# Performance work log

Measured on AMD Instinct MI355X. Metric: run time of the kernel, lower is better.

Reference implementation:

```python
import jax, jax.numpy as jnp
import numpy as np
from jax import lax

N_STATES = 512
VOCAB = 32000
BATCH = 16
SEQ_LEN = 128


def setup_inputs() -> dict:
    key = jax.random.key(0)
    k_ids, k_em, k_tm, k_p = jax.random.split(key, 4)
    input_ids = jax.random.randint(k_ids, (BATCH, SEQ_LEN), 0, VOCAB, dtype=jnp.int64)
    em = jax.random.normal(k_em, (N_STATES, VOCAB), dtype=jnp.float32)
    tm = jax.random.normal(k_tm, (N_STATES, N_STATES), dtype=jnp.float32)
    p = jax.random.normal(k_p, (N_STATES,), dtype=jnp.float32)
    return {"input_ids": input_ids, "em": em, "tm": tm, "p": p}


def reference(input_ids, em, tm, p):
    """HMM forward algorithm in log space; returns mean NLL (scalar).

    em: [S, V] emission logits, tm: [S, S] transition logits, p: [S] prior logits.
    do_log_softmax=True -> normalize each in log space first.
    """
    log_em = jax.nn.log_softmax(em, axis=-1)   # [S, V]
    log_tm = jax.nn.log_softmax(tm, axis=-1)   # [S, S] rows = source state
    log_p = jax.nn.log_softmax(p, axis=-1)     # [S]

    # Gather emission log-probs per token: [B, T, S]
    em_tok = log_em.T[input_ids]

    # alpha_0[b, s] = log_p[s] + log_em[s, x_0]
    alpha0 = log_p[None, :] + em_tok[:, 0]     # [B, S]

    def step(alpha, e_t):
        # alpha: [B, S_src]; log-matmul: logsumexp over source states
        a = jax.nn.logsumexp(alpha[:, :, None] + log_tm[None, :, :], axis=1) + e_t
        return a, None

    em_rest = jnp.swapaxes(em_tok[:, 1:], 0, 1)  # [T-1, B, S]
    alpha_T, _ = lax.scan(step, alpha0, em_rest)

    # loss = -mean_b log p(x_b) = -mean_b logsumexp_s alpha_T[b, s]
    loss = -jnp.mean(jax.nn.logsumexp(alpha_T, axis=-1))
    return loss
```

## Files before the change

kernel.cpp:

```cpp
#include <hip/hip_runtime.h>
#include <hip/hip_bf16.h>

#define NS 512
#define NV 32000
#define NB 16
#define NT 128

#ifndef __has_builtin
#define __has_builtin(x) 0
#endif

typedef int v8i __attribute__((ext_vector_type(8)));
typedef float v4f __attribute__((ext_vector_type(4)));

__device__ inline unsigned enc_e4m3(float x) {
    x = fminf(x, 448.0f);
    unsigned u = __float_as_uint(x);
    if (x < 0.015625f) {
        return (unsigned)(int)rintf(x * 512.0f);
    }
    unsigned u2 = u + 0x7FFFFu + ((u >> 20) & 1u);
    return (((u2 >> 23) - 120u) << 3) | ((u2 >> 20) & 7u);
}

__device__ inline unsigned pack4_e4m3(float a, float b, float c, float d) {
#if __has_builtin(__builtin_amdgcn_cvt_pk_fp8_f32)
    int v = __builtin_amdgcn_cvt_pk_fp8_f32(a, b, 0, false);
    v = __builtin_amdgcn_cvt_pk_fp8_f32(c, d, v, true);
    return (unsigned)v;
#else
    return enc_e4m3(a) | (enc_e4m3(b) << 8) | (enc_e4m3(c) << 16) | (enc_e4m3(d) << 24);
#endif
}

#define DPPMAX(x, ctrl) \
    x = fmaxf(x, __int_as_float(__builtin_amdgcn_mov_dpp(__float_as_int(x), ctrl, 0xF, 0xF, true)))
#define DPPADD(x, ctrl) \
    x = x + __int_as_float(__builtin_amdgcn_mov_dpp(__float_as_int(x), ctrl, 0xF, 0xF, true))

__global__ __launch_bounds__(256) void k_emtok_T(
    const float* __restrict__ em, const int* __restrict__ ids,
    float* __restrict__ em_lin_T)
{
    const int s   = blockIdx.x;
    const int tid = threadIdx.x;
    const float* row = em + (size_t)s * NV;

    float sum = 0.f;
    const float4* row4 = (const float4*)row;
#pragma unroll 4
    for (int i = 0; i < 31; ++i) {
        float4 v = row4[tid + 256 * i];
        sum += __expf(v.x) + __expf(v.y) + __expf(v.z) + __expf(v.w);
    }
    sum += __expf(row[31744 + tid]);

#pragma unroll
    for (int off = 32; off; off >>= 1) sum += __shfl_down(sum, off);
    __shared__ float red[4];
    __shared__ float s_scale;
    if ((tid & 63) == 0) red[tid >> 6] = sum;
    __syncthreads();
    if (tid == 0) s_scale = (1.0f / ((red[0] + red[1]) + (red[2] + red[3]))) * 0x1p-18f;
    __syncthreads();
    const float scale = s_scale;

    for (int j = tid; j < NB * NT; j += 256) {
        em_lin_T[(size_t)s * (NB * NT) + j] = __expf(row[ids[j]]) * scale;
    }
}

__global__ __launch_bounds__(256) void k_emtok_direct(
    const float* __restrict__ em, const int* __restrict__ ids,
    float* __restrict__ em_lin)
{
    const int s   = blockIdx.x;
    const int tid = threadIdx.x;
    const float* row = em + (size_t)s * NV;

    float sum = 0.f;
    const float4* row4 = (const float4*)row;
#pragma unroll 4
    for (int i = 0; i < 31; ++i) {
        float4 v = row4[tid + 256 * i];
        sum += __expf(v.x) + __expf(v.y) + __expf(v.z) + __expf(v.w);
    }
    sum += __expf(row[31744 + tid]);
#pragma unroll
    for (int off = 32; off; off >>= 1) sum += __shfl_down(sum, off);
    __shared__ float red[4];
    __shared__ float s_scale;
    if ((tid & 63) == 0) red[tid >> 6] = sum;
    __syncthreads();
    if (tid == 0) s_scale = (1.0f / ((red[0] + red[1]) + (red[2] + red[3]))) * 0x1p-18f;
    __syncthreads();
    const float scale = s_scale;
    for (int j = tid; j < NB * NT; j += 256) {
        em_lin[(size_t)j * NS + s] = __expf(row[ids[j]]) * scale;
    }
}

__global__ __launch_bounds__(256) void k_tr(
    const float* __restrict__ emT, float* __restrict__ em_lin)
{
    __shared__ float tile[32][33];
    const int jb = blockIdx.x * 32;
    const int sb = blockIdx.y * 32;
    const int cc = threadIdx.x & 31;
    const int rr = threadIdx.x >> 5;
#pragma unroll
    for (int i = 0; i < 4; ++i) {
        int r = rr + 8 * i;
        tile[r][cc] = emT[(size_t)(sb + r) * (NB * NT) + jb + cc];
    }
    __syncthreads();
#pragma unroll
    for (int i = 0; i < 4; ++i) {
        int r = rr + 8 * i;
        em_lin[(size_t)(jb + r) * NS + sb + cc] = tile[cc][r];
    }
}

__global__ __launch_bounds__(64) void k_pt(
    const float* __restrict__ tm, unsigned char* __restrict__ PT)
{
    const int k    = blockIdx.x;
    const int lane = threadIdx.x;
    const float* row = tm + (size_t)k * NS;

    float4 a = ((const float4*)row)[lane * 2];
    float4 b = ((const float4*)row)[lane * 2 + 1];
    float e0 = __expf(a.x), e1 = __expf(a.y), e2 = __expf(a.z), e3 = __expf(a.w);
    float e4 = __expf(b.x), e5 = __expf(b.y), e6 = __expf(b.z), e7 = __expf(b.w);
    float sum = ((e0 + e1) + (e2 + e3)) + ((e4 + e5) + (e6 + e7));
#pragma unroll
    for (int off = 32; off; off >>= 1) sum += __shfl_down(sum, off);
    sum = __shfl(sum, 0);
    const float sc = 1024.0f / sum;

    float ev[8] = {e0, e1, e2, e3, e4, e5, e6, e7};
#pragma unroll
    for (int i = 0; i < 8; ++i) {
        int d = lane * 8 + i;
        PT[(size_t)d * NS + k] = (unsigned char)(pack4_e4m3(ev[i] * sc, 0.f, 0.f, 0.f) & 0xFFu);
    }
}

__global__ __launch_bounds__(512, 2) void k_scan(
    const float* __restrict__ em_lin, const unsigned char* __restrict__ PT,
    const float* __restrict__ p, float* __restrict__ out)
{
    const int tid = threadIdx.x;
    const int w   = tid >> 6;
    const int l   = tid & 63;
    const int lc  = l & 15;
    const int lq  = l >> 4;

    __shared__ unsigned int Ew[2][16 * 128];
    __shared__ float wm[16][8];
    __shared__ float mbuf[16];
    __shared__ int   sbuf[16];

    v8i B[4][4];
#pragma unroll
    for (int nt = 0; nt < 4; ++nt) {
#pragma unroll
        for (int kt = 0; kt < 4; ++kt) {
            const uint4* src = (const uint4*)(PT + (size_t)((w * 4 + nt) * 16 + lc) * NS + kt * 128 + lq * 32);
            uint4 lo = src[0], hi = src[1];
            v8i bb;
            bb[0] = (int)lo.x; bb[1] = (int)lo.y; bb[2] = (int)lo.z; bb[3] = (int)lo.w;
            bb[4] = (int)hi.x; bb[5] = (int)hi.y; bb[6] = (int)hi.z; bb[7] = (int)hi.w;
            B[nt][kt] = bb;
        }
    }

    float zp = 0.f;
#pragma unroll
    for (int i = 0; i < 8; ++i) zp += __expf(p[l * 8 + i]);
    DPPADD(zp, 0x111); DPPADD(zp, 0x112); DPPADD(zp, 0x114); DPPADD(zp, 0x118);
    float Zp = __int_as_float(__builtin_amdgcn_readlane(__float_as_int(zp), 15))
             + __int_as_float(__builtin_amdgcn_readlane(__float_as_int(zp), 31))
             + __int_as_float(__builtin_amdgcn_readlane(__float_as_int(zp), 47))
             + __int_as_float(__builtin_amdgcn_readlane(__float_as_int(zp), 63));
    const float invZp = 1.0f / Zp;

    int dbase[4];
#pragma unroll
    for (int nt = 0; nt < 4; ++nt) dbase[nt] = (w * 4 + nt) * 16 + lc;

    float alpha[4][4];
#pragma unroll
    for (int nt = 0; nt < 4; ++nt) {
        float pl = __expf(p[dbase[nt]]) * invZp;
#pragma unroll
        for (int r = 0; r < 4; ++r)
            alpha[nt][r] = pl * em_lin[(4 * lq + r) * (NT * NS) + dbase[nt]];
    }

    int shift[4] = {0, 0, 0, 0};
    const unsigned sel1 = (l & 1) ? 0x07030501u : 0x02060004u;
    const unsigned sel2 = (l & 2) ? 0x07060302u : 0x01000504u;
    const int mrow = 4 * lq + (l & 3);

    for (int t = 1; t < NT; ++t) {
        float epf[4][4];
#pragma unroll
        for (int nt = 0; nt < 4; ++nt)
#pragma unroll
            for (int r = 0; r < 4; ++r)
                epf[nt][r] = em_lin[(4 * lq + r) * (NT * NS) + t * NS + dbase[nt]];

#pragma unroll
        for (int r = 0; r < 4; ++r) {
            float mx = fmaxf(fmaxf(alpha[0][r], alpha[1][r]), fmaxf(alpha[2][r], alpha[3][r]));
            DPPMAX(mx, 0x111); DPPMAX(mx, 0x112); DPPMAX(mx, 0x114); DPPMAX(mx, 0x118);
            if (lc == 15) wm[4 * lq + r][w] = mx;
        }
        __syncthreads();
        if (w == 0 && l < 16) {
            float4 a = *(const float4*)&wm[l][0];
            float4 b = *(const float4*)&wm[l][4];
            mbuf[l] = fmaxf(fmaxf(fmaxf(a.x, a.y), fmaxf(a.z, a.w)),
                            fmaxf(fmaxf(b.x, b.y), fmaxf(b.z, b.w)));
        }
        __syncthreads();
        float4 mb4 = *(const float4*)&mbuf[4 * lq];
        float mbv[4] = {mb4.x, mb4.y, mb4.z, mb4.w};
        float sc[4];
#pragma unroll
        for (int r = 0; r < 4; ++r) {
            int Eb = (int)(__float_as_uint(mbv[r]) >> 23);
            sc[r] = __uint_as_float((unsigned)(261 - Eb) << 23);
            shift[r] += Eb - 126;
        }
#pragma unroll
        for (int nt = 0; nt < 4; ++nt) {
            unsigned dw = pack4_e4m3(alpha[nt][0] * sc[0], alpha[nt][1] * sc[1],
                                     alpha[nt][2] * sc[2], alpha[nt][3] * sc[3]);
            int tmp = __builtin_amdgcn_mov_dpp((int)dw, 0xB1, 0xF, 0xF, true);
            dw = __builtin_amdgcn_perm(dw, (unsigned)tmp, sel1);
            tmp = __builtin_amdgcn_mov_dpp((int)dw, 0x4E, 0xF, 0xF, true);
            dw = __builtin_amdgcn_perm(dw, (unsigned)tmp, sel2);
            int chunk = ((w * 4 + nt) ^ mrow) & 31;
            Ew[t & 1][mrow * 128 + chunk * 4 + (lc >> 2)] = dw;
        }
        __syncthreads();

        v8i A[4];
        const uint4* eb = (const uint4*)&Ew[t & 1][0];
#pragma unroll
        for (int kt = 0; kt < 4; ++kt) {
            uint4 lo = eb[lc * 32 + (((kt * 8 + lq * 2 + 0) ^ lc) & 31)];
            uint4 hi = eb[lc * 32 + (((kt * 8 + lq * 2 + 1) ^ lc) & 31)];
            v8i aa;
            aa[0] = (int)lo.x; aa[1] = (int)lo.y; aa[2] = (int)lo.z; aa[3] = (int)lo.w;
            aa[4] = (int)hi.x; aa[5] = (int)hi.y; aa[6] = (int)hi.z; aa[7] = (int)hi.w;
            A[kt] = aa;
        }

        v4f C[4];
#pragma unroll
        for (int nt = 0; nt < 4; ++nt) { C[nt][0] = 0.f; C[nt][1] = 0.f; C[nt][2] = 0.f; C[nt][3] = 0.f; }
#pragma unroll
        for (int kt = 0; kt < 4; ++kt)
#pragma unroll
            for (int nt = 0; nt < 4; ++nt)
                C[nt] = __builtin_amdgcn_mfma_scale_f32_16x16x128_f8f6f4(
                            A[kt], B[nt][kt], C[nt], 0, 0, 0, 0x7F7F7F7F, 0, 0x7F7F7F7F);

#pragma unroll
        for (int nt = 0; nt < 4; ++nt)
#pragma unroll
            for (int r = 0; r < 4; ++r)
                alpha[nt][r] = C[nt][r] * epf[nt][r];
    }

#pragma unroll
    for (int r = 0; r < 4; ++r) {
        float sm = ((alpha[0][r] + alpha[1][r]) + (alpha[2][r] + alpha[3][r]));
        DPPADD(sm, 0x111); DPPADD(sm, 0x112); DPPADD(sm, 0x114); DPPADD(sm, 0x118);
        if (lc == 15) wm[4 * lq + r][w] = sm;
        if (w == 0 && lc == 0) sbuf[4 * lq + r] = shift[r];
    }
    __syncthreads();
    if (w == 0 && l < 16) {
        float4 a = *(const float4*)&wm[l][0];
        float4 b = *(const float4*)&wm[l][4];
        float s8 = ((a.x + a.y) + (a.z + a.w)) + ((b.x + b.y) + (b.z + b.w));
        float L2 = __log2f(s8) + (float)sbuf[l];
        DPPADD(L2, 0x111); DPPADD(L2, 0x112); DPPADD(L2, 0x114); DPPADD(L2, 0x118);
        if (l == 15) out[0] = -(0.693147180559945f / 16.0f) * L2;
    }
}

extern "C" void kernel_launch(void* const* d_in, const int* in_sizes, int n_in,
                              void* d_out, int out_size, void* d_ws, size_t ws_size,
                              hipStream_t stream)
{
    const int*   ids = (const int*)d_in[0];
    const float* em  = (const float*)d_in[1];
    const float* tm  = (const float*)d_in[2];
    const float* p   = (const float*)d_in[3];
    float* out = (float*)d_out;

    float*          em_lin = (float*)d_ws;
    unsigned char*  PT     = (unsigned char*)d_ws + ((size_t)4 << 20);
    float*          emT    = (float*)((unsigned char*)d_ws + ((size_t)4 << 20) + ((size_t)256 << 10));

    const bool big_ws = ws_size >= (((size_t)8 << 20) + ((size_t)512 << 10));

    if (big_ws) {
        k_emtok_T<<<NS, 256, 0, stream>>>(em, ids, emT);
        k_tr<<<dim3(64, 16), 256, 0, stream>>>(emT, em_lin);
    } else {
        k_emtok_direct<<<NS, 256, 0, stream>>>(em, ids, em_lin);
    }
    k_pt<<<NS, 64, 0, stream>>>(tm, PT);
    k_scan<<<1, 512, 0, stream>>>(em_lin, PT, p, out);
}
```

Before: 295.7 us.

## Drop a scan barrier per step, coalesce PT build, prefetch emission gathers

In the serial scan, every thread now reads all eight per-warp maxima from shared memory and reduces them itself, which removes one __syncthreads per timestep. The Ew exchange buffer becomes single-buffered, and the emission pointers are advanced incrementally instead of being recomputed. The transition-matrix fp8 transpose is split into a row-normaliser kernel and a tiled kernel that writes coalesced 16-byte stores, replacing byte-wise strided writes. The emission gather values are loaded before the softmax-sum loop so their latency overlaps it. The trade-offs are one extra kernel launch and redundant max reductions in every thread, and the initial shift value changes to 18.

```diff
diff --git a/kernel.cpp b/kernel.cpp
--- a/kernel.cpp
+++ b/kernel.cpp
@@ -46,6 +46,13 @@
     const int tid = threadIdx.x;
     const float* row = em + (size_t)s * NV;
 
+    int idv[8];
+#pragma unroll
+    for (int k = 0; k < 8; ++k) idv[k] = ids[tid + 256 * k];
+    float g[8];
+#pragma unroll
+    for (int k = 0; k < 8; ++k) g[k] = row[idv[k]];
+
     float sum = 0.f;
     const float4* row4 = (const float4*)row;
 #pragma unroll 4
@@ -65,9 +72,9 @@
     __syncthreads();
     const float scale = s_scale;
 
-    for (int j = tid; j < NB * NT; j += 256) {
-        em_lin_T[(size_t)s * (NB * NT) + j] = __expf(row[ids[j]]) * scale;
-    }
+#pragma unroll
+    for (int k = 0; k < 8; ++k)
+        em_lin_T[(size_t)s * (NB * NT) + tid + 256 * k] = __expf(g[k]) * scale;
 }
 
 __global__ __launch_bounds__(256) void k_emtok_direct(
@@ -77,6 +84,13 @@
     const int s   = blockIdx.x;
     const int tid = threadIdx.x;
     const float* row = em + (size_t)s * NV;
+
+    int idv[8];
+#pragma unroll
+    for (int k = 0; k < 8; ++k) idv[k] = ids[tid + 256 * k];
+    float g[8];
+#pragma unroll
+    for (int k = 0; k < 8; ++k) g[k] = row[idv[k]];
 
     float sum = 0.f;
     const float4* row4 = (const float4*)row;
@@ -95,9 +109,9 @@
     if (tid == 0) s_scale = (1.0f / ((red[0] + red[1]) + (red[2] + red[3]))) * 0x1p-18f;
     __syncthreads();
     const float scale = s_scale;
-    for (int j = tid; j < NB * NT; j += 256) {
-        em_lin[(size_t)j * NS + s] = __expf(row[ids[j]]) * scale;
-    }
+#pragma unroll
+    for (int k = 0; k < 8; ++k)
+        em_lin[(size_t)(tid + 256 * k) * NS + s] = __expf(g[k]) * scale;
 }
 
 __global__ __launch_bounds__(256) void k_tr(
@@ -121,8 +135,8 @@
     }
 }
 
-__global__ __launch_bounds__(64) void k_pt(
-    const float* __restrict__ tm, unsigned char* __restrict__ PT)
+__global__ __launch_bounds__(64) void k_z(
+    const float* __restrict__ tm, float* __restrict__ zscale)
 {
     const int k    = blockIdx.x;
     const int lane = threadIdx.x;
@@ -130,20 +144,46 @@
 
     float4 a = ((const float4*)row)[lane * 2];
     float4 b = ((const float4*)row)[lane * 2 + 1];
-    float e0 = __expf(a.x), e1 = __expf(a.y), e2 = __expf(a.z), e3 = __expf(a.w);
-    float e4 = __expf(b.x), e5 = __expf(b.y), e6 = __expf(b.z), e7 = __expf(b.w);
-    float sum = ((e0 + e1) + (e2 + e3)) + ((e4 + e5) + (e6 + e7));
+    float sum = ((__expf(a.x) + __expf(a.y)) + (__expf(a.z) + __expf(a.w)))
+              + ((__expf(b.x) + __expf(b.y)) + (__expf(b.z) + __expf(b.w)));
 #pragma unroll
     for (int off = 32; off; off >>= 1) sum += __shfl_down(sum, off);
-    sum = __shfl(sum, 0);
-    const float sc = 1024.0f / sum;
-
-    float ev[8] = {e0, e1, e2, e3, e4, e5, e6, e7};
-#pragma unroll
-    for (int i = 0; i < 8; ++i) {
-        int d = lane * 8 + i;
-        PT[(size_t)d * NS + k] = (unsigned char)(pack4_e4m3(ev[i] * sc, 0.f, 0.f, 0.f) & 0xFFu);
-    }
+    if (lane == 0) zscale[k] = 1024.0f / sum;
+}
+
+__global__ __launch_bounds__(256) void k_pt2(
+    const float* __restrict__ tm, const float* __restrict__ zscale,
+    unsigned char* __restrict__ PT)
+{
+    __shared__ float tile[64][65];
+    __shared__ float zs[64];
+    const int kb  = blockIdx.x * 64;
+    const int db  = blockIdx.y * 64;
+    const int tid = threadIdx.x;
+    const int c   = tid & 63;
+    const int r0  = tid >> 6;
+
+    if (tid < 64) zs[tid] = zscale[kb + tid];
+#pragma unroll
+    for (int i = 0; i < 16; ++i) {
+        int r = r0 + 4 * i;
+        tile[r][c] = tm[(size_t)(kb + r) * NS + db + c];
+    }
+    __syncthreads();
+
+    const int d  = tid >> 2;
+    const int ks = (tid & 3) * 16;
+    unsigned px[4];
+#pragma unroll
+    for (int gq = 0; gq < 4; ++gq) {
+        int k0 = ks + gq * 4;
+        px[gq] = pack4_e4m3(__expf(tile[k0 + 0][d]) * zs[k0 + 0],
+                            __expf(tile[k0 + 1][d]) * zs[k0 + 1],
+                            __expf(tile[k0 + 2][d]) * zs[k0 + 2],
+                            __expf(tile[k0 + 3][d]) * zs[k0 + 3]);
+    }
+    uint4 o; o.x = px[0]; o.y = px[1]; o.z = px[2]; o.w = px[3];
+    *(uint4*)(PT + (size_t)(db + d) * NS + kb + ks) = o;
 }
 
 __global__ __launch_bounds__(512, 2) void k_scan(
@@ -156,9 +196,8 @@
     const int lc  = l & 15;
     const int lq  = l >> 4;
 
-    __shared__ unsigned int Ew[2][16 * 128];
-    __shared__ float wm[16][8];
-    __shared__ float mbuf[16];
+    __shared__ unsigned int Ew[16 * 128];
+    __shared__ float wm2[8][16];
     __shared__ int   sbuf[16];
 
     v8i B[4][4];
@@ -185,48 +224,65 @@
              + __int_as_float(__builtin_amdgcn_readlane(__float_as_int(zp), 63));
     const float invZp = 1.0f / Zp;
 
-    int dbase[4];
-#pragma unroll
-    for (int nt = 0; nt < 4; ++nt) dbase[nt] = (w * 4 + nt) * 16 + lc;
+    const int dbase0 = w * 64 + lc;
 
     float alpha[4][4];
 #pragma unroll
     for (int nt = 0; nt < 4; ++nt) {
-        float pl = __expf(p[dbase[nt]]) * invZp;
+        float pl = __expf(p[dbase0 + 16 * nt]) * invZp;
 #pragma unroll
         for (int r = 0; r < 4; ++r)
-            alpha[nt][r] = pl * em_lin[(4 * lq + r) * (NT * NS) + dbase[nt]];
-    }
-
-    int shift[4] = {0, 0, 0, 0};
+            alpha[nt][r] = pl * em_lin[(4 * lq + r) * (NT * NS) + dbase0 + 16 * nt];
+    }
+
+    int shift[4] = {18, 18, 18, 18};
     const unsigned sel1 = (l & 1) ? 0x07030501u : 0x02060004u;
     const unsigned sel2 = (l & 2) ? 0x07060302u : 0x01000504u;
     const int mrow = 4 * lq + (l & 3);
 
+    const float* ep[4];
+#pragma unroll
+    for (int r = 0; r < 4; ++r)
+        ep[r] = em_lin + (size_t)(4 * lq + r) * (NT * NS) + NS + dbase0;
+
     for (int t = 1; t < NT; ++t) {
         float epf[4][4];
 #pragma unroll
         for (int nt = 0; nt < 4; ++nt)
 #pragma unroll
             for (int r = 0; r < 4; ++r)
-                epf[nt][r] = em_lin[(4 * lq + r) * (NT * NS) + t * NS + dbase[nt]];
+                epf[nt][r] = ep[r][16 * nt];
+#pragma unroll
+        for (int r = 0; r < 4; ++r) ep[r] += NS;
 
 #pragma unroll
         for (int r = 0; r < 4; ++r) {
             float mx = fmaxf(fmaxf(alpha[0][r], alpha[1][r]), fmaxf(alpha[2][r], alpha[3][r]));
             DPPMAX(mx, 0x111); DPPMAX(mx, 0x112); DPPMAX(mx, 0x114); DPPMAX(mx, 0x118);
-            if (lc == 15) wm[4 * lq + r][w] = mx;
+            if (lc == 15) wm2[w][4 * lq + r] = mx;
         }
         __syncthreads();
-        if (w == 0 && l < 16) {
-            float4 a = *(const float4*)&wm[l][0];
-            float4 b = *(const float4*)&wm[l][4];
-            mbuf[l] = fmaxf(fmaxf(fmaxf(a.x, a.y), fmaxf(a.z, a.w)),
-                            fmaxf(fmaxf(b.x, b.y), fmaxf(b.z, b.w)));
-        }
-        __syncthreads();
-        float4 mb4 = *(const float4*)&mbuf[4 * lq];
-        float mbv[4] = {mb4.x, mb4.y, mb4.z, mb4.w};
+
+        float4 M4;
+        {
+            float4 v0 = *(const float4*)&wm2[0][4 * lq];
+            float4 v1 = *(const float4*)&wm2[1][4 * lq];
+            float4 v2 = *(const float4*)&wm2[2][4 * lq];
+            float4 v3 = *(const float4*)&wm2[3][4 * lq];
+            float4 v4 = *(const float4*)&wm2[4][4 * lq];
+            float4 v5 = *(const float4*)&wm2[5][4 * lq];
+            float4 v6 = *(const float4*)&wm2[6][4 * lq];
+            float4 v7 = *(const float4*)&wm2[7][4 * lq];
+            M4.x = fmaxf(fmaxf(fmaxf(v0.x, v1.x), fmaxf(v2.x, v3.x)),
+                         fmaxf(fmaxf(v4.x, v5.x), fmaxf(v6.x, v7.x)));
+            M4.y = fmaxf(fmaxf(fmaxf(v0.y, v1.y), fmaxf(v2.y, v3.y)),
+                         fmaxf(fmaxf(v4.y, v5.y), fmaxf(v6.y, v7.y)));
+            M4.z = fmaxf(fmaxf(fmaxf(v0.z, v1.z), fmaxf(v2.z, v3.z)),
+                         fmaxf(fmaxf(v4.z, v5.z), fmaxf(v6.z, v7.z)));
+            M4.w = fmaxf(fmaxf(fmaxf(v0.w, v1.w), fmaxf(v2.w, v3.w)),
+                         fmaxf(fmaxf(v4.w, v5.w), fmaxf(v6.w, v7.w)));
+        }
+        float mbv[4] = {M4.x, M4.y, M4.z, M4.w};
         float sc[4];
 #pragma unroll
         for (int r = 0; r < 4; ++r) {
@@ -234,6 +290,7 @@
             sc[r] = __uint_as_float((unsigned)(261 - Eb) << 23);
             shift[r] += Eb - 126;
         }
+
 #pragma unroll
         for (int nt = 0; nt < 4; ++nt) {
             unsigned dw = pack4_e4m3(alpha[nt][0] * sc[0], alpha[nt][1] * sc[1],
@@ -243,12 +300,12 @@
             tmp = __builtin_amdgcn_mov_dpp((int)dw, 0x4E, 0xF, 0xF, true);
             dw = __builtin_amdgcn_perm(dw, (unsigned)tmp, sel2);
             int chunk = ((w * 4 + nt) ^ mrow) & 31;
-            Ew[t & 1][mrow * 128 + chunk * 4 + (lc >> 2)] = dw;
+            Ew[mrow * 128 + chunk * 4 + (lc >> 2)] = dw;
         }
         __syncthreads();
 
         v8i A[4];
-        const uint4* eb = (const uint4*)&Ew[t & 1][0];
+        const uint4* eb = (const uint4*)&Ew[0];
 #pragma unroll
         for (int kt = 0; kt < 4; ++kt) {
             uint4 lo = eb[lc * 32 + (((kt * 8 + lq * 2 + 0) ^ lc) & 31)];
@@ -280,14 +337,14 @@
     for (int r = 0; r < 4; ++r) {
         float sm = ((alpha[0][r] + alpha[1][r]) + (alpha[2][r] + alpha[3][r]));
         DPPADD(sm, 0x111); DPPADD(sm, 0x112); DPPADD(sm, 0x114); DPPADD(sm, 0x118);
-        if (lc == 15) wm[4 * lq + r][w] = sm;
+        if (lc == 15) wm2[w][4 * lq + r] = sm;
         if (w == 0 && lc == 0) sbuf[4 * lq + r] = shift[r];
     }
     __syncthreads();
     if (w == 0 && l < 16) {
-        float4 a = *(const float4*)&wm[l][0];
-        float4 b = *(const float4*)&wm[l][4];
-        float s8 = ((a.x + a.y) + (a.z + a.w)) + ((b.x + b.y) + (b.z + b.w));
+        float s8 = 0.f;
+#pragma unroll
+        for (int j = 0; j < 8; ++j) s8 += wm2[j][l];
         float L2 = __log2f(s8) + (float)sbuf[l];
         DPPADD(L2, 0x111); DPPADD(L2, 0x112); DPPADD(L2, 0x114); DPPADD(L2, 0x118);
         if (l == 15) out[0] = -(0.693147180559945f / 16.0f) * L2;
@@ -306,7 +363,8 @@
 
     float*          em_lin = (float*)d_ws;
     unsigned char*  PT     = (unsigned char*)d_ws + ((size_t)4 << 20);
-    float*          emT    = (float*)((unsigned char*)d_ws + ((size_t)4 << 20) + ((size_t)256 << 10));
+    float*          zscale = (float*)((unsigned char*)d_ws + ((size_t)4 << 20) + ((size_t)256 << 10));
+    float*          emT    = (float*)((unsigned char*)d_ws + ((size_t)4 << 20) + ((size_t)512 << 10));
 
     const bool big_ws = ws_size >= (((size_t)8 << 20) + ((size_t)512 << 10));
 
@@ -316,6 +374,7 @@
     } else {
         k_emtok_direct<<<NS, 256, 0, stream>>>(em, ids, em_lin);
     }
-    k_pt<<<NS, 64, 0, stream>>>(tm, PT);
+    k_z<<<NS, 64, 0, stream>>>(tm, zscale);
+    k_pt2<<<dim3(8, 8), 256, 0, stream>>>(tm, zscale, PT);
     k_scan<<<1, 512, 0, stream>>>(em_lin, PT, p, out);
 }
```

New measurement: 309.7 us. +4.7%, slower.
